# Performance work log

Hardware: AMD Instinct MI355X
Metric: run time of the kernel (lower is better)

## Reference

```python
import jax, jax.numpy as jnp
import numpy as np

MAX_LENGTH = 41
SOS_index = 0


def setup_inputs() -> dict:
    key = jax.random.key(0)
    ks = jax.random.split(key, 16)
    B, S, H, V = 32, 41, 1024, 16384
    sc = 0.02
    inp = {
        "encoder_outputs": jax.random.normal(ks[0], (B, S, H), jnp.float32),
        "encoder_hidden": jax.random.normal(ks[1], (1, B, H), jnp.float32),
        "target_tensor": jax.random.randint(ks[2], (B, MAX_LENGTH), 0, V, jnp.int64),
        # embedding table
        "emb": jax.random.normal(ks[3], (V, H), jnp.float32) * sc,
        # Bahdanau attention params
        "Wq": jax.random.normal(ks[4], (H, H), jnp.float32) * sc,
        "bq": jnp.zeros((H,), jnp.float32),
        "Wk": jax.random.normal(ks[5], (H, H), jnp.float32) * sc,
        "bk": jnp.zeros((H,), jnp.float32),
        "Vw": jax.random.normal(ks[6], (1, H), jnp.float32) * sc,
        "bV": jnp.zeros((1,), jnp.float32),
        # LSTM params (PyTorch gate order: i, f, g, o)
        "Wih": jax.random.normal(ks[7], (4 * H, 2 * H), jnp.float32) * sc,
        "Whh": jax.random.normal(ks[8], (4 * H, H), jnp.float32) * sc,
        "bih": jnp.zeros((4 * H,), jnp.float32),
        "bhh": jnp.zeros((4 * H,), jnp.float32),
        # output projection
        "Wout": jax.random.normal(ks[9], (V, H), jnp.float32) * sc,
        "bout": jnp.zeros((V,), jnp.float32),
    }
    return inp


def reference(encoder_outputs, encoder_hidden, target_tensor, emb,
              Wq, bq, Wk, bk, Vw, bV, Wih, Whh, bih, bhh, Wout, bout):
    B = encoder_outputs.shape[0]
    H = encoder_outputs.shape[2]
    # keys projection is invariant across decode steps
    keys_proj = jnp.einsum('bsh,gh->bsg', encoder_outputs, Wk) + bk  # [B,S,H]
    # teacher-forced input tokens: SOS then target[:, :-1]
    sos = jnp.full((1, B), SOS_index, dtype=target_tensor.dtype)
    tokens = jnp.concatenate([sos, target_tensor.T[:-1]], axis=0)  # [T,B]

    h0 = encoder_hidden[0]            # [B,H]
    c0 = jnp.zeros_like(h0)

    def step(carry, tok):
        h, c = carry
        x = emb[tok]                                       # [B,H] (dropout: eval mode)
        q = h @ Wq.T + bq                                  # [B,H] query from hidden
        e = jnp.tanh(q[:, None, :] + keys_proj)            # [B,S,H]
        scores = jnp.einsum('bsh,h->bs', e, Vw[0]) + bV[0] # [B,S]
        w = jax.nn.softmax(scores, axis=-1)                # [B,S]
        ctx = jnp.einsum('bs,bsh->bh', w, encoder_outputs) # [B,H]
        xi = jnp.concatenate([x, ctx], axis=-1)            # [B,2H]
        gates = xi @ Wih.T + h @ Whh.T + (bih + bhh)       # [B,4H]
        i_g, f_g, g_g, o_g = jnp.split(gates, 4, axis=-1)
        i_g = jax.nn.sigmoid(i_g)
        f_g = jax.nn.sigmoid(f_g)
        g_g = jnp.tanh(g_g)
        o_g = jax.nn.sigmoid(o_g)
        c_new = f_g * c + i_g * g_g
        h_new = o_g * jnp.tanh(c_new)
        logits = h_new @ Wout.T + bout                     # [B,V]
        return (h_new, c_new), (logits, w)

    (h_f, c_f), (logits, attn) = jax.lax.scan(step, (h0, c0), tokens)
    decoder_outputs = jax.nn.log_softmax(logits.transpose(1, 0, 2), axis=-1)  # [B,T,V]
    attentions = attn.transpose(1, 0, 2)                                       # [B,T,S]
    return decoder_outputs, h_f[None], c_f[None], attentions
```

## Files before the change

kernel.cpp:

```cpp
#include <hip/hip_runtime.h>
#include <hip/hip_bf16.h>
#include <math.h>

#define B 32
#define S 41
#define T 41
#define H 1024
#define V 16384
#define BH (B*H)
#define NBLK 256
#define NTHR 512
#define RPB 20

typedef unsigned int uint;
typedef unsigned short ushort;
typedef __attribute__((ext_vector_type(8))) short bf16x8;
typedef __attribute__((ext_vector_type(4))) float f32x4;
typedef _Float16 h2v __attribute__((ext_vector_type(2)));

__device__ __forceinline__ float fast_sigmoid(float x){ return 1.f/(1.f + __expf(-x)); }
__device__ __forceinline__ float fast_tanh(float x){
  float e = __expf(-2.f*fabsf(x));
  float r = (1.f - e)/(1.f + e);
  return copysignf(r, x);
}
__device__ __forceinline__ ushort f2h(float f){ return __builtin_bit_cast(unsigned short, (_Float16)f); }
__device__ __forceinline__ float h2f(ushort u){ return (float)__builtin_bit_cast(_Float16, u); }
__device__ __forceinline__ h2v bc2(uint u){ return __builtin_bit_cast(h2v, u); }
__device__ __forceinline__ ushort f2bf(float f){
  uint u = __float_as_uint(f);
  u = u + 0x7FFFu + ((u>>16)&1u);
  return (ushort)(u>>16);
}

#if defined(__has_builtin)
#if __has_builtin(__builtin_amdgcn_fdot2)
#define HAS_FDOT2 1
#endif
#endif
__device__ __forceinline__ float dot2(h2v a, h2v b, float c){
#ifdef HAS_FDOT2
  return __builtin_amdgcn_fdot2(a, b, c, false);
#else
  return fmaf((float)a.x, (float)b.x, fmaf((float)a.y, (float)b.y, c));
#endif
}

__device__ __forceinline__ void ldx8_sc(const uint* p, uint4* r){
  asm volatile(
    "global_load_dwordx4 %0, %8, off sc0 sc1\n\t"
    "global_load_dwordx4 %1, %8, off offset:16 sc0 sc1\n\t"
    "global_load_dwordx4 %2, %8, off offset:32 sc0 sc1\n\t"
    "global_load_dwordx4 %3, %8, off offset:48 sc0 sc1\n\t"
    "global_load_dwordx4 %4, %8, off offset:64 sc0 sc1\n\t"
    "global_load_dwordx4 %5, %8, off offset:80 sc0 sc1\n\t"
    "global_load_dwordx4 %6, %8, off offset:96 sc0 sc1\n\t"
    "global_load_dwordx4 %7, %8, off offset:112 sc0 sc1\n\t"
    "s_waitcnt vmcnt(0)"
    : "=&v"(r[0]), "=&v"(r[1]), "=&v"(r[2]), "=&v"(r[3]),
      "=&v"(r[4]), "=&v"(r[5]), "=&v"(r[6]), "=&v"(r[7])
    : "v"(p) : "memory");
}
__device__ __forceinline__ void ld_qgh_sc(const float* qp, const float* gp,
                                          float4* q, float* gh){
  asm volatile(
    "global_load_dwordx4 %0, %5, off sc0 sc1\n\t"
    "global_load_dwordx4 %1, %5, off offset:16 sc0 sc1\n\t"
    "global_load_dwordx4 %2, %5, off offset:32 sc0 sc1\n\t"
    "global_load_dwordx4 %3, %5, off offset:48 sc0 sc1\n\t"
    "global_load_dword  %4, %6, off sc0 sc1\n\t"
    "s_waitcnt vmcnt(0)"
    : "=&v"(q[0]), "=&v"(q[1]), "=&v"(q[2]), "=&v"(q[3]), "=&v"(*gh)
    : "v"(qp), "v"(gp) : "memory");
}
__device__ __forceinline__ void st_sc_f32(float* p, float v){
  asm volatile("global_store_dword %0, %1, off sc0 sc1" :: "v"(p), "v"(v) : "memory");
}

__device__ __forceinline__ void gbar_full(uint* bar, int phase){
  asm volatile("s_waitcnt vmcnt(0)" ::: "memory");
  __syncthreads();
  if (threadIdx.x == 0){
    const int gid = blockIdx.x >> 5;
    __builtin_amdgcn_fence(__ATOMIC_RELEASE, "agent");
    uint old = __hip_atomic_fetch_add(&bar[gid*32], 1u, __ATOMIC_RELAXED, __HIP_MEMORY_SCOPE_AGENT);
    if ((old & 31u) == 31u){
      uint r = __hip_atomic_fetch_add(&bar[256], 1u, __ATOMIC_RELAXED, __HIP_MEMORY_SCOPE_AGENT);
      if ((r & 7u) == 7u){
        #pragma unroll
        for (int g = 0; g < 8; ++g)
          __hip_atomic_store(&bar[288+g*32], (uint)phase, __ATOMIC_RELAXED, __HIP_MEMORY_SCOPE_AGENT);
      }
    }
    while (__hip_atomic_load(&bar[288+gid*32], __ATOMIC_RELAXED, __HIP_MEMORY_SCOPE_AGENT) < (uint)phase)
      __builtin_amdgcn_s_sleep(2);
  }
  __syncthreads();
}

__device__ __forceinline__ void gbar_x(uint* bar, int phase,
                                       uint my_xcd, uint my_cnt, uint nx, uint lb){
  asm volatile("s_waitcnt vmcnt(0)" ::: "memory");
  __syncthreads();
  if (threadIdx.x == 0){
    uint old = __hip_atomic_fetch_add(&bar[512 + my_xcd*16], 1u, __ATOMIC_RELAXED, __HIP_MEMORY_SCOPE_AGENT);
    if (old == lb*my_cnt + (my_cnt - 1u)){
      __builtin_amdgcn_fence(__ATOMIC_RELEASE, "agent");
      uint r = __hip_atomic_fetch_add(&bar[640], 1u, __ATOMIC_RELAXED, __HIP_MEMORY_SCOPE_AGENT);
      if (r == lb*nx + (nx - 1u)){
        #pragma unroll
        for (int g = 0; g < 8; ++g)
          __hip_atomic_store(&bar[704+g*16], (uint)phase, __ATOMIC_RELAXED, __HIP_MEMORY_SCOPE_AGENT);
      }
    }
    while (__hip_atomic_load(&bar[704+my_xcd*16], __ATOMIC_RELAXED, __HIP_MEMORY_SCOPE_AGENT) < (uint)phase)
      __builtin_amdgcn_s_sleep(2);
  }
  __syncthreads();
}

__global__ __launch_bounds__(256) void k_init(const float* __restrict__ eh,
                                              ushort* __restrict__ h16, uint* __restrict__ bar){
  int i = blockIdx.x*256 + threadIdx.x;
  h16[i] = f2h(eh[i]);
  if (i < 1024) bar[i] = 0;
}

__global__ __launch_bounds__(256) void k_bsum(const float* __restrict__ a,
                                              const float* __restrict__ b, float* __restrict__ o){
  int i = blockIdx.x*256 + threadIdx.x;
  o[i] = a[i] + b[i];
}

__global__ __launch_bounds__(256) void k_gather(const float* __restrict__ emb,
    const int* __restrict__ tgt, float* __restrict__ Xall){
  int r = blockIdx.x;
  int t = r / B, b = r % B;
  int tok = (t==0) ? 0 : tgt[b*T + (t-1)];
  const float4* src = (const float4*)(emb + (size_t)tok*H);
  float4* dst = (float4*)(Xall + (size_t)r*H);
  dst[threadIdx.x] = src[threadIdx.x];
}

__global__ __launch_bounds__(256) void k_cvt16(const float* __restrict__ src,
                                               ushort* __restrict__ dst, int n8){
  int i = blockIdx.x*256 + threadIdx.x;
  if (i >= n8) return;
  const float4* s4 = (const float4*)src + (size_t)i*2;
  float4 a = s4[0], b = s4[1];
  union { ushort us[8]; uint4 v; } p;
  p.us[0]=f2h(a.x); p.us[1]=f2h(a.y); p.us[2]=f2h(a.z); p.us[3]=f2h(a.w);
  p.us[4]=f2h(b.x); p.us[5]=f2h(b.y); p.us[6]=f2h(b.z); p.us[7]=f2h(b.w);
  ((uint4*)dst)[i] = p.v;
}

__global__ __launch_bounds__(256) void k_bgemm(const float* __restrict__ A,
    const float* __restrict__ W, const float* __restrict__ bias, float* __restrict__ C,
    int M, int N, int wstride, int woff)
{
  __shared__ ushort As[128*40];
  __shared__ ushort Bs[128*40];
  const int tid = threadIdx.x;
  const int n0 = blockIdx.x*128, m0 = blockIdx.y*128;
  const int row = tid>>1, half = tid&1;
  const int lane = tid & 63, widx = tid >> 6;
  const int wm = (widx>>1)*64, wn = (widx&1)*64;

  int arow = m0 + row; if (arow > M-1) arow = M-1;
  const float* ga = A + (size_t)arow*1024 + half*16;
  const float* gw = W + (size_t)(n0+row)*wstride + woff + half*16;
  ushort* sa = &As[row*40 + half*16];
  ushort* sb = &Bs[row*40 + half*16];

  f32x4 acc[4][4] = {};

  for (int k0 = 0; k0 < 1024; k0 += 32) {
    float4 a0 = *(const float4*)(ga+k0),   a1 = *(const float4*)(ga+k0+4);
    float4 a2 = *(const float4*)(ga+k0+8), a3 = *(const float4*)(ga+k0+12);
    float4 w0 = *(const float4*)(gw+k0),   w1 = *(const float4*)(gw+k0+4);
    float4 w2 = *(const float4*)(gw+k0+8), w3 = *(const float4*)(gw+k0+12);
    __syncthreads();
    {
      union { ushort us[8]; uint4 v; } p, q;
      p.us[0]=f2bf(a0.x); p.us[1]=f2bf(a0.y); p.us[2]=f2bf(a0.z); p.us[3]=f2bf(a0.w);
      p.us[4]=f2bf(a1.x); p.us[5]=f2bf(a1.y); p.us[6]=f2bf(a1.z); p.us[7]=f2bf(a1.w);
      q.us[0]=f2bf(a2.x); q.us[1]=f2bf(a2.y); q.us[2]=f2bf(a2.z); q.us[3]=f2bf(a2.w);
      q.us[4]=f2bf(a3.x); q.us[5]=f2bf(a3.y); q.us[6]=f2bf(a3.z); q.us[7]=f2bf(a3.w);
      *(uint4*)sa = p.v; *(uint4*)(sa+8) = q.v;
      p.us[0]=f2bf(w0.x); p.us[1]=f2bf(w0.y); p.us[2]=f2bf(w0.z); p.us[3]=f2bf(w0.w);
      p.us[4]=f2bf(w1.x); p.us[5]=f2bf(w1.y); p.us[6]=f2bf(w1.z); p.us[7]=f2bf(w1.w);
      q.us[0]=f2bf(w2.x); q.us[1]=f2bf(w2.y); q.us[2]=f2bf(w2.z); q.us[3]=f2bf(w2.w);
      q.us[4]=f2bf(w3.x); q.us[5]=f2bf(w3.y); q.us[6]=f2bf(w3.z); q.us[7]=f2bf(w3.w);
      *(uint4*)sb = p.v; *(uint4*)(sb+8) = q.v;
    }
    __syncthreads();
    bf16x8 af[4], bf[4];
    #pragma unroll
    for (int i=0;i<4;i++)
      af[i] = *(const bf16x8*)&As[(wm + i*16 + (lane&15))*40 + (lane>>4)*8];
    #pragma unroll
    for (int j=0;j<4;j++)
      bf[j] = *(const bf16x8*)&Bs[(wn + j*16 + (lane&15))*40 + (lane>>4)*8];
    #pragma unroll
    for (int i=0;i<4;i++)
      #pragma unroll
      for (int j=0;j<4;j++)
        acc[i][j] = __builtin_amdgcn_mfma_f32_16x16x32_bf16(af[i], bf[j], acc[i][j], 0, 0, 0);
  }

  #pragma unroll
  for (int i=0;i<4;i++){
    #pragma unroll
    for (int j=0;j<4;j++){
      int n = n0 + wn + j*16 + (lane&15);
      float bv = bias ? bias[n] : 0.f;
      #pragma unroll
      for (int qq=0;qq<4;qq++){
        int m = m0 + wm + i*16 + ((lane>>4)<<2) + qq;
        if (m < M) C[(size_t)m*N + n] = acc[i][j][qq] + bv;
      }
    }
  }
}

__global__ __launch_bounds__(512, 2) void k_loop(
    const ushort* __restrict__ Wc16,
    const float* __restrict__ bq,
    const ushort* __restrict__ keys16,
    const float* __restrict__ Vw, const float* __restrict__ bV,
    const float* __restrict__ GxF,
    const ushort* __restrict__ encW16,
    float* __restrict__ qg,
    float* __restrict__ ghg,
    ushort* __restrict__ h16,
    float* __restrict__ hhist,
    float* __restrict__ attn_out,
    float* __restrict__ hf, float* __restrict__ cf,
    uint* __restrict__ bar)
{
  __shared__ __align__(16) uint   w_lds[RPB*516];
  __shared__ __align__(16) ushort ew_lds[512*42];
  __shared__ __align__(16) float  red[RPB*512];
  __shared__ float sc_sh[64];
  __shared__ float ga[512];

  const int tid = threadIdx.x;
  const int bid = blockIdx.x;
  const int pb_b = bid >> 3, pb_mc = bid & 7;
  const int lane = tid & 63, wv = tid >> 6;

  const int pa_b = tid & 31, pa_ks = tid >> 5;
  const int gn = (tid >> 7)*H + pb_mc*128 + (tid & 127);

  const int na = bid*RPB + (tid>>5);
  const int nb = bid*RPB + 16 + (tid>>5);
  const float bqa = (na < H) ? bq[na] : 0.f;
  const float bqb = (tid < 128 && nb < H) ? bq[nb] : 0.f;

  uint my_xcd = 0, my_cnt = 0, nx = 8, lb = 0;
  if (tid == 0){
    uint x;
    asm volatile("s_getreg_b32 %0, hwreg(20, 0, 32)" : "=s"(x));
    my_xcd = x & 7u;
    __hip_atomic_fetch_add(&bar[832 + my_xcd*16], 1u, __ATOMIC_RELAXED, __HIP_MEMORY_SCOPE_AGENT);
  }

  for (int i = tid; i < RPB*128; i += NTHR){
    int r = i >> 7, j = i & 127;
    uint4 v = *((const uint4*)(Wc16 + (size_t)(bid*RPB + r)*1024) + j);
    *(uint4*)&w_lds[r*516 + j*4] = v;
  }
  for (int s = 0; s < S; ++s)
    ew_lds[tid*42 + s] = encW16[((size_t)pb_b*S + s)*4096 + gn];
  float vreg[16];
  {
    const float4* vp = (const float4*)(Vw + lane*16);
    *(float4*)&vreg[0] = vp[0]; *(float4*)&vreg[4]  = vp[1];
    *(float4*)&vreg[8] = vp[2]; *(float4*)&vreg[12] = vp[3];
  }
  const float bV0 = bV[0];
  float creg = 0.f;
  __syncthreads();

  for (int t = 0; t < T; ++t) {
    {
      uint4 hr[8];
      ldx8_sc((const uint*)h16 + pa_b*512 + pa_ks*32, hr);
      float part[RPB];
      #pragma unroll
      for (int r = 0; r < RPB; ++r){
        const uint* wr = &w_lds[r*516 + pa_ks*32];
        float a0 = 0.f, a1 = 0.f;
        #pragma unroll
        for (int j = 0; j < 8; ++j){
          uint4 w = *(const uint4*)(wr + j*4);
          uint4 h = hr[j];
          a0 = dot2(bc2(w.x), bc2(h.x), a0);
          a1 = dot2(bc2(w.y), bc2(h.y), a1);
          a0 = dot2(bc2(w.z), bc2(h.z), a0);
          a1 = dot2(bc2(w.w), bc2(h.w), a1);
        }
        part[r] = a0 + a1;
      }
      #pragma unroll
      for (int r = 0; r < RPB; ++r) red[r*512 + pa_ks*32 + pa_b] = part[r];
      __syncthreads();
      {
        int r = tid >> 5, b2 = tid & 31;
        const float* rp = &red[r*512 + b2];
        float s = 0.f;
        #pragma unroll
        for (int k2 = 0; k2 < 16; ++k2) s += rp[k2*32];
        if (na < H) qg[b2*H + na] = s + bqa;
        else        ghg[(size_t)b2*4*H + (na - H)] = s;
      }
      if (tid < 128){
        int r = 16 + (tid >> 5), b2 = tid & 31;
        const float* rp = &red[r*512 + b2];
        float s = 0.f;
        #pragma unroll
        for (int k2 = 0; k2 < 16; ++k2) s += rp[k2*32];
        if (nb < H) qg[b2*H + nb] = s + bqb;
        else        ghg[(size_t)b2*4*H + (nb - H)] = s;
      }
    }
    if (t == 0){
      gbar_full(bar, 1);
      if (tid == 0){
        my_cnt = __hip_atomic_load(&bar[832 + my_xcd*16], __ATOMIC_RELAXED, __HIP_MEMORY_SCOPE_AGENT);
        uint n = 0;
        #pragma unroll
        for (int g = 0; g < 8; ++g)
          n += (__hip_atomic_load(&bar[832 + g*16], __ATOMIC_RELAXED, __HIP_MEMORY_SCOPE_AGENT) != 0u) ? 1u : 0u;
        nx = n;
      }
    } else {
      gbar_x(bar, 2*t + 1, my_xcd, my_cnt, nx, lb); lb++;
    }

    {
      float4 q4[4]; float ghv;
      ld_qgh_sc(qg + pb_b*H + lane*16, ghg + (size_t)pb_b*4*H + gn, q4, &ghv);
      float gxv = GxF[((size_t)t*B + pb_b)*4*H + gn];
      float qarr[16];
      *(float4*)&qarr[0] = q4[0]; *(float4*)&qarr[4]  = q4[1];
      *(float4*)&qarr[8] = q4[2]; *(float4*)&qarr[12] = q4[3];

      for (int s = wv; s < S; s += 8) {
        const ushort* kr = keys16 + ((size_t)pb_b*S + s)*H + lane*16;
        uint4 k0 = *(const uint4*)kr;
        uint4 k1 = *(const uint4*)(kr + 8);
        float part = 0.f;
        #define SC2(u, e) { h2v hh = bc2(u); \
          part += fast_tanh(qarr[e]   + (float)hh.x) * vreg[e]; \
          part += fast_tanh(qarr[e+1] + (float)hh.y) * vreg[e+1]; }
        SC2(k0.x,0) SC2(k0.y,2) SC2(k0.z,4) SC2(k0.w,6)
        SC2(k1.x,8) SC2(k1.y,10) SC2(k1.z,12) SC2(k1.w,14)
        #undef SC2
        #pragma unroll
        for (int off = 32; off > 0; off >>= 1) part += __shfl_xor(part, off);
        if (lane == 0) sc_sh[s] = part + bV0;
      }
      __syncthreads();
      if (tid < 64) {
        float val = (tid < S) ? sc_sh[tid] : -1e30f;
        float m = val;
        #pragma unroll
        for (int off = 32; off > 0; off >>= 1) m = fmaxf(m, __shfl_xor(m, off));
        float e = (tid < S) ? __expf(val - m) : 0.f;
        float ssum = e;
        #pragma unroll
        for (int off = 32; off > 0; off >>= 1) ssum += __shfl_xor(ssum, off);
        if (tid < S) {
          float w = e / ssum;
          sc_sh[tid] = w;
          if (pb_mc == 0) st_sc_f32(&attn_out[((size_t)pb_b*T + t)*S + tid], w);
        }
      }
      __syncthreads();
      {
        float acc = gxv + ghv;
        const ushort* ep = &ew_lds[tid*42];
        #pragma unroll
        for (int s = 0; s < S; ++s)
          acc = fmaf(sc_sh[s], h2f(ep[s]), acc);
        ga[tid] = acc;
      }
      __syncthreads();
      if (tid < 128) {
        float ig = fast_sigmoid(ga[tid]);
        float fg = fast_sigmoid(ga[128+tid]);
        float gg = fast_tanh   (ga[256+tid]);
        float og = fast_sigmoid(ga[384+tid]);
        creg = fg*creg + ig*gg;
        float hn = og * fast_tanh(creg);
        int m = pb_mc*128 + tid;
        h16[pb_b*H + m] = f2h(hn);
        st_sc_f32(&hhist[((size_t)pb_b*T + t)*H + m], hn);
        if (t == T-1) { hf[pb_b*H + m] = hn; cf[pb_b*H + m] = creg; }
      }
    }
    if (t < T-1) { gbar_x(bar, 2*t + 2, my_xcd, my_cnt, nx, lb); lb++; }
  }
}

__global__ __launch_bounds__(256) void k_logsm(float* __restrict__ p_all)
{
  float* p = p_all + (size_t)blockIdx.x * V;
  const int tid = threadIdx.x;
  const int lane = tid & 63, wave = tid >> 6;
  __shared__ float red[4];
  float4 v[16];
  float m = -1e30f;
  #pragma unroll
  for (int j=0;j<16;j++){
    v[j] = *(const float4*)(p + 4*(tid + 256*j));
    m = fmaxf(m, fmaxf(fmaxf(v[j].x, v[j].y), fmaxf(v[j].z, v[j].w)));
  }
  #pragma unroll
  for (int off=32; off>0; off>>=1) m = fmaxf(m, __shfl_xor(m, off));
  if (lane==0) red[wave] = m;
  __syncthreads();
  m = fmaxf(fmaxf(red[0], red[1]), fmaxf(red[2], red[3]));
  float ssum = 0.f;
  #pragma unroll
  for (int j=0;j<16;j++){
    ssum += __expf(v[j].x - m) + __expf(v[j].y - m) + __expf(v[j].z - m) + __expf(v[j].w - m);
  }
  #pragma unroll
  for (int off=32; off>0; off>>=1) ssum += __shfl_xor(ssum, off);
  __syncthreads();
  if (lane==0) red[wave] = ssum;
  __syncthreads();
  float lse = m + __logf(red[0] + red[1] + red[2] + red[3]);
  #pragma unroll
  for (int j=0;j<16;j++){
    float4 o; o.x = v[j].x - lse; o.y = v[j].y - lse; o.z = v[j].z - lse; o.w = v[j].w - lse;
    *(float4*)(p + 4*(tid + 256*j)) = o;
  }
}

extern "C" void kernel_launch(void* const* d_in, const int* in_sizes, int n_in,
                              void* d_out, int out_size, void* d_ws, size_t ws_size,
                              hipStream_t stream) {
  const float* enc   = (const float*)d_in[0];
  const float* ehid  = (const float*)d_in[1];
  const int*   tgt   = (const int*)  d_in[2];
  const float* emb   = (const float*)d_in[3];
  const float* Wq    = (const float*)d_in[4];
  const float* bq    = (const float*)d_in[5];
  const float* Wk    = (const float*)d_in[6];
  const float* bk    = (const float*)d_in[7];
  const float* Vw    = (const float*)d_in[8];
  const float* bV    = (const float*)d_in[9];
  const float* Wih   = (const float*)d_in[10];
  const float* Whh   = (const float*)d_in[11];
  const float* bih   = (const float*)d_in[12];
  const float* bhh   = (const float*)d_in[13];
  const float* Wout  = (const float*)d_in[14];
  const float* bout  = (const float*)d_in[15];

  float* out  = (float*)d_out;
  float* dec  = out;
  float* hf   = out + (size_t)B*T*V;
  float* cf   = hf + BH;
  float* attn = cf + BH;

  float*  Xall   = dec;
  float*  keysF  = dec +  1343488;
  float*  GxF    = dec +  2686976;
  float*  encWF  = dec +  8060928;
  ushort* keys16 = (ushort*)(dec + 13434880);
  ushort* encW16 = (ushort*)(dec + 14106624);
  ushort* Wc16   = (ushort*)(dec + 16793600);

  float* ws = (float*)d_ws;
  float*  hhist = ws;
  float*  bsum  = ws + 1343488;
  ushort* h16   = (ushort*)(ws + 1347584);
  float*  qg    = ws + 1363968;
  float*  ghg   = ws + 1396736;
  uint*   bar   = (uint*)(ws + 1527808);

  k_init<<<BH/256, 256, 0, stream>>>(ehid, h16, bar);
  k_bsum<<<(4*H)/256, 256, 0, stream>>>(bih, bhh, bsum);
  k_gather<<<T*B, 256, 0, stream>>>(emb, tgt, Xall);

  { dim3 g(H/128, 11);     k_bgemm<<<g, 256, 0, stream>>>(enc,  Wk,  bk,     keysF, B*S, H,   H,   0); }
  { dim3 g((4*H)/128, 11); k_bgemm<<<g, 256, 0, stream>>>(Xall, Wih, bsum,   GxF,   T*B, 4*H, 2*H, 0); }
  { dim3 g((4*H)/128, 11); k_bgemm<<<g, 256, 0, stream>>>(enc,  Wih, nullptr,encWF, B*S, 4*H, 2*H, H); }

  k_cvt16<<<(B*S*H/8 + 255)/256, 256, 0, stream>>>(keysF, keys16, B*S*H/8);
  k_cvt16<<<(B*S*4*H/8 + 255)/256, 256, 0, stream>>>(encWF, encW16, B*S*4*H/8);
  k_cvt16<<<(H*H/8 + 255)/256, 256, 0, stream>>>(Wq,  Wc16,             H*H/8);
  k_cvt16<<<(4*H*H/8 + 255)/256, 256, 0, stream>>>(Whh, Wc16 + (size_t)H*H, 4*H*H/8);

  {
    void* kargs[] = {
      (void*)&Wc16, (void*)&bq, (void*)&keys16, (void*)&Vw, (void*)&bV,
      (void*)&GxF, (void*)&encW16, (void*)&qg, (void*)&ghg,
      (void*)&h16, (void*)&hhist, (void*)&attn, (void*)&hf, (void*)&cf, (void*)&bar
    };
    hipLaunchCooperativeKernel((const void*)k_loop, dim3(NBLK), dim3(NTHR), kargs, 0, stream);
  }

  { dim3 g(V/128, 11);     k_bgemm<<<g, 256, 0, stream>>>(hhist, Wout, bout, dec, B*T, V, H, 0); }
  k_logsm<<<B*T, 256, 0, stream>>>(dec);
}
```

Measured before the change: 1.283 ms.

## Publish cross-block state via atomic swaps and drop barrier release fence

Cross-block values (q, gh, h16) are now published with device-scope atomic exchanges instead of plain or sc0/sc1 stores, and h16 is packed two halves per 32-bit word through LDS. This lets the release fence in the per-XCD grid barrier be removed, the barrier spin sleep is shortened, and the GxF load is hoisted ahead of the barrier. Attention and hidden-history outputs switch to plain and nontemporal stores. The aim is to cut grid-barrier latency on the serial 41-step recurrence. The risk is memory-ordering correctness without the fence, plus extra atomic traffic.

```diff
diff --git a/kernel.cpp b/kernel.cpp
--- a/kernel.cpp
+++ b/kernel.cpp
@@ -44,6 +44,13 @@
 #else
   return fmaf((float)a.x, (float)b.x, fmaf((float)a.y, (float)b.y, c));
 #endif
+}
+
+__device__ __forceinline__ float at_sw_f32(float* p, float v){
+  return __hip_atomic_exchange(p, v, __ATOMIC_RELAXED, __HIP_MEMORY_SCOPE_AGENT);
+}
+__device__ __forceinline__ uint at_sw_u32(uint* p, uint v){
+  return __hip_atomic_exchange(p, v, __ATOMIC_RELAXED, __HIP_MEMORY_SCOPE_AGENT);
 }
 
 __device__ __forceinline__ void ldx8_sc(const uint* p, uint4* r){
@@ -73,9 +80,6 @@
     : "=&v"(q[0]), "=&v"(q[1]), "=&v"(q[2]), "=&v"(q[3]), "=&v"(*gh)
     : "v"(qp), "v"(gp) : "memory");
 }
-__device__ __forceinline__ void st_sc_f32(float* p, float v){
-  asm volatile("global_store_dword %0, %1, off sc0 sc1" :: "v"(p), "v"(v) : "memory");
-}
 
 __device__ __forceinline__ void gbar_full(uint* bar, int phase){
   asm volatile("s_waitcnt vmcnt(0)" ::: "memory");
@@ -105,7 +109,6 @@
   if (threadIdx.x == 0){
     uint old = __hip_atomic_fetch_add(&bar[512 + my_xcd*16], 1u, __ATOMIC_RELAXED, __HIP_MEMORY_SCOPE_AGENT);
     if (old == lb*my_cnt + (my_cnt - 1u)){
-      __builtin_amdgcn_fence(__ATOMIC_RELEASE, "agent");
       uint r = __hip_atomic_fetch_add(&bar[640], 1u, __ATOMIC_RELAXED, __HIP_MEMORY_SCOPE_AGENT);
       if (r == lb*nx + (nx - 1u)){
         #pragma unroll
@@ -114,7 +117,7 @@
       }
     }
     while (__hip_atomic_load(&bar[704+my_xcd*16], __ATOMIC_RELAXED, __HIP_MEMORY_SCOPE_AGENT) < (uint)phase)
-      __builtin_amdgcn_s_sleep(2);
+      __builtin_amdgcn_s_sleep(1);
   }
   __syncthreads();
 }
@@ -243,11 +246,13 @@
   __shared__ __align__(16) float  red[RPB*512];
   __shared__ float sc_sh[64];
   __shared__ float ga[512];
+  __shared__ float hsh[128];
 
   const int tid = threadIdx.x;
   const int bid = blockIdx.x;
   const int pb_b = bid >> 3, pb_mc = bid & 7;
   const int lane = tid & 63, wv = tid >> 6;
+  uint* h16u = (uint*)h16;
 
   const int pa_b = tid & 31, pa_ks = tid >> 5;
   const int gn = (tid >> 7)*H + pb_mc*128 + (tid & 127);
@@ -256,6 +261,8 @@
   const int nb = bid*RPB + 16 + (tid>>5);
   const float bqa = (na < H) ? bq[na] : 0.f;
   const float bqb = (tid < 128 && nb < H) ? bq[nb] : 0.f;
+
+  float adum = 0.f; uint udum = 0u;
 
   uint my_xcd = 0, my_cnt = 0, nx = 8, lb = 0;
   if (tid == 0){
@@ -283,9 +290,10 @@
   __syncthreads();
 
   for (int t = 0; t < T; ++t) {
+    float gxv;
     {
       uint4 hr[8];
-      ldx8_sc((const uint*)h16 + pa_b*512 + pa_ks*32, hr);
+      ldx8_sc((const uint*)h16u + pa_b*512 + pa_ks*32, hr);
       float part[RPB];
       #pragma unroll
       for (int r = 0; r < RPB; ++r){
@@ -311,8 +319,8 @@
         float s = 0.f;
         #pragma unroll
         for (int k2 = 0; k2 < 16; ++k2) s += rp[k2*32];
-        if (na < H) qg[b2*H + na] = s + bqa;
-        else        ghg[(size_t)b2*4*H + (na - H)] = s;
+        if (na < H) adum += at_sw_f32(&qg[b2*H + na], s + bqa);
+        else        adum += at_sw_f32(&ghg[(size_t)b2*4*H + (na - H)], s);
       }
       if (tid < 128){
         int r = 16 + (tid >> 5), b2 = tid & 31;
@@ -320,9 +328,10 @@
         float s = 0.f;
         #pragma unroll
         for (int k2 = 0; k2 < 16; ++k2) s += rp[k2*32];
-        if (nb < H) qg[b2*H + nb] = s + bqb;
-        else        ghg[(size_t)b2*4*H + (nb - H)] = s;
-      }
+        if (nb < H) adum += at_sw_f32(&qg[b2*H + nb], s + bqb);
+        else        adum += at_sw_f32(&ghg[(size_t)b2*4*H + (nb - H)], s);
+      }
+      gxv = GxF[((size_t)t*B + pb_b)*4*H + gn];
     }
     if (t == 0){
       gbar_full(bar, 1);
@@ -341,7 +350,6 @@
     {
       float4 q4[4]; float ghv;
       ld_qgh_sc(qg + pb_b*H + lane*16, ghg + (size_t)pb_b*4*H + gn, q4, &ghv);
-      float gxv = GxF[((size_t)t*B + pb_b)*4*H + gn];
       float qarr[16];
       *(float4*)&qarr[0] = q4[0]; *(float4*)&qarr[4]  = q4[1];
       *(float4*)&qarr[8] = q4[2]; *(float4*)&qarr[12] = q4[3];
@@ -374,7 +382,7 @@
         if (tid < S) {
           float w = e / ssum;
           sc_sh[tid] = w;
-          if (pb_mc == 0) st_sc_f32(&attn_out[((size_t)pb_b*T + t)*S + tid], w);
+          if (pb_mc == 0) attn_out[((size_t)pb_b*T + t)*S + tid] = w;
         }
       }
       __syncthreads();
@@ -395,13 +403,21 @@
         creg = fg*creg + ig*gg;
         float hn = og * fast_tanh(creg);
         int m = pb_mc*128 + tid;
-        h16[pb_b*H + m] = f2h(hn);
-        st_sc_f32(&hhist[((size_t)pb_b*T + t)*H + m], hn);
+        hsh[tid] = hn;
+        __builtin_nontemporal_store(hn, &hhist[((size_t)pb_b*T + t)*H + m]);
         if (t == T-1) { hf[pb_b*H + m] = hn; cf[pb_b*H + m] = creg; }
       }
+      __syncthreads();
+      if (tid < 64) {
+        uint pk = (uint)f2h(hsh[2*tid]) | ((uint)f2h(hsh[2*tid+1]) << 16);
+        udum |= at_sw_u32(&h16u[(size_t)pb_b*512 + pb_mc*64 + tid], pk);
+      }
     }
     if (t < T-1) { gbar_x(bar, 2*t + 2, my_xcd, my_cnt, nx, lb); lb++; }
   }
+
+  if (__float_as_uint(adum) + udum == 0x1234567u)
+    __hip_atomic_store(&bar[1020], udum, __ATOMIC_RELAXED, __HIP_MEMORY_SCOPE_AGENT);
 }
 
 __global__ __launch_bounds__(256) void k_logsm(float* __restrict__ p_all)
```

Measured after the change: 1.410 ms. +9.9%, slower.
